# Optimization experiments

Measured on AMD Instinct MI355X. Metric: run time of the kernel, lower is better.

The kernel has to match this reference:

```python
import jax, jax.numpy as jnp
import numpy as np

N_WIRES = 16
VAR_DEPTH = 2
BATCH = 16


def _param_sizes():
    sizes = []
    n = N_WIRES
    lay = 0
    while n > 1:
        sizes.append(4 * int(np.ceil(N_WIRES / 2 ** lay)) * VAR_DEPTH)
        n = (n + 1) // 2
        lay += 1
    return sizes  # [128, 64, 32, 16]


def _apply_1q(psi, gate, w):
    # psi: (B, 2, ..., 2); gate: (2,2) complex; wire w lives on axis w+1
    psi = jnp.moveaxis(psi, w + 1, -1)
    psi = jnp.einsum('...j,ij->...i', psi, gate)
    return jnp.moveaxis(psi, -1, w + 1)


def _rx(psi, th, w):
    c = jnp.cos(th / 2).astype(jnp.complex64)
    s = jnp.sin(th / 2).astype(jnp.complex64)
    gate = jnp.stack([jnp.stack([c, -1j * s]), jnp.stack([-1j * s, c])])
    return _apply_1q(psi, gate, w)


def _rz(psi, th, w):
    ph = jnp.exp(0.5j * th * jnp.array([-1.0, 1.0], jnp.float32)).astype(jnp.complex64)
    shape = [1] * psi.ndim
    shape[w + 1] = 2
    return psi * ph.reshape(shape)


def _rzz(psi, th, wa, wb):
    # diag(e^{-i t/2}, e^{i t/2}, e^{i t/2}, e^{-i t/2}) -> sign = -1 if bits equal else +1
    sgn = jnp.array([[-1.0, 1.0], [1.0, -1.0]], jnp.float32)
    ph = jnp.exp(0.5j * th * sgn).astype(jnp.complex64)  # symmetric, transpose-safe
    a, b = min(wa, wb) + 1, max(wa, wb) + 1
    shape = [1] * psi.ndim
    shape[a] = 2
    shape[b] = 2
    return psi * ph.reshape(shape)


def _cnot(psi, c, t):
    p0 = jax.lax.slice_in_dim(psi, 0, 1, axis=c + 1)
    p1 = jax.lax.slice_in_dim(psi, 1, 2, axis=c + 1)
    return jnp.concatenate([p0, jnp.flip(p1, axis=t + 1)], axis=c + 1)


def _conv_layer(psi, params, active):
    n = len(active)
    for d in range(VAR_DEPTH):
        for j in range(n):
            base = 4 * j + d * 4 * n
            psi = _rx(psi, params[base + 0], active[j])
            psi = _rz(psi, params[base + 1], active[j])
            psi = _rx(psi, params[base + 2], active[j])
        for bg in (0, 1):
            for j in range(bg, n, 2):
                jn = (j + 1) % n  # ring coupling (wraps last->first)
                base = 4 * j + d * 4 * n
                psi = _rzz(psi, params[base + 3], active[j], active[jn])
    return psi


def _pool(psi, active):
    for j in range(0, len(active), 2):
        if j + 1 < len(active):
            psi = _cnot(psi, active[j], active[j + 1])
    return psi, active[::2]


def _forward(psi, params_list):
    active = list(range(N_WIRES))
    for p in params_list:
        psi = _conv_layer(psi, p, active)
        if len(active) > 1:
            psi, active = _pool(psi, active)
    w = active[0]  # measure Z on the surviving wire (wire 0)
    prob = psi.real ** 2 + psi.imag ** 2
    axes = tuple(a for a in range(1, psi.ndim) if a != w + 1)
    p2 = prob.sum(axis=axes)  # (B, 2)
    return p2[:, 0] - p2[:, 1]


def setup_inputs() -> dict:
    key = jax.random.key(0)
    ks = jax.random.split(key, 8)
    dim = 2 ** N_WIRES
    x_re = jax.random.normal(ks[0], (BATCH, dim), dtype=jnp.float32)
    x_im = jax.random.normal(ks[1], (BATCH, dim), dtype=jnp.float32)
    nrm = jnp.sqrt(jnp.sum(x_re ** 2 + x_im ** 2, axis=1, keepdims=True))
    x_re = x_re / nrm
    x_im = x_im / nrm
    sizes = _param_sizes()
    two_pi = 2.0 * np.pi
    params = [jax.random.uniform(ks[2 + i], (sizes[i],), dtype=jnp.float32) * two_pi
              for i in range(len(sizes))]
    return {"x_re": x_re, "x_im": x_im,
            "params0": params[0], "params1": params[1],
            "params2": params[2], "params3": params[3]}


def reference(x_re, x_im, params0, params1, params2, params3):
    psi = (x_re + 1j * x_im).astype(jnp.complex64)
    psi = psi.reshape((BATCH,) + (2,) * N_WIRES)
    return _forward(psi, [params0, params1, params2, params3])
```

## Files before the change

### kernel.cpp

```cpp
#include <hip/hip_runtime.h>


#define DEV __device__ __forceinline__
#define TBL(i) (tbl + (i)*8)

__device__ static const unsigned char G_CP[60] = {
  15,14,13,12,11,10,9,8,7,6,5,4,3,2,1,0,
  15,14,13,12,11,10,9,8,7,6,5,4,3,2,1,0,
  15,13,11,9,7,5,3,1,
  15,13,11,9,7,5,3,1,
  15,11,7,3,
  15,11,7,3,
  15,7,
  15,7
};
__device__ static const unsigned char G_CQ[60] = {
  14,13,12,11,10,9,8,7,6,5,4,3,2,1,0,15,
  14,13,12,11,10,9,8,7,6,5,4,3,2,1,0,15,
  13,11,9,7,5,3,1,15,
  13,11,9,7,5,3,1,15,
  11,7,3,15,
  11,7,3,15,
  7,15,
  7,15
};

DEV float2 F2(float x, float y){ float2 r; r.x = x; r.y = y; return r; }
DEV float2 cmulf(float2 a, float2 b){ return F2(a.x*b.x - a.y*b.y, a.x*b.y + a.y*b.x); }
DEV int swz(int j){ return j ^ ((j>>4)&15) ^ ((j>>8)&15); }

template<int SB>
DEV void gate4(float2* a, const float* __restrict__ g){
  float u00r=g[0],u00i=g[1],u01r=g[2],u01i=g[3],u10r=g[4],u10i=g[5],u11r=g[6],u11i=g[7];
  #pragma unroll
  for (int m=0;m<2;m++){
    int i0 = (SB==0) ? (m<<1) : m;
    int i1 = i0 | (1<<SB);
    float2 x0=a[i0], x1=a[i1];
    a[i0] = F2(u00r*x0.x - u00i*x0.y + u01r*x1.x - u01i*x1.y,
               u00r*x0.y + u00i*x0.x + u01r*x1.y + u01i*x1.x);
    a[i1] = F2(u10r*x0.x - u10i*x0.y + u11r*x1.x - u11i*x1.y,
               u10r*x0.y + u10i*x0.x + u11r*x1.y + u11i*x1.x);
  }
}

DEV void lgate(float2* a, const float* __restrict__ g, int mask, int lane){
  bool h = (lane & mask) != 0;
  float c0r = h ? g[4] : g[0], c0i = h ? g[5] : g[1];
  float c1r = h ? g[6] : g[2], c1i = h ? g[7] : g[3];
  #pragma unroll
  for (int s=0;s<4;s++){
    float px = __shfl_xor(a[s].x, mask);
    float py = __shfl_xor(a[s].y, mask);
    float x0x = h ? px : a[s].x, x0y = h ? py : a[s].y;
    float x1x = h ? a[s].x : px, x1y = h ? a[s].y : py;
    a[s] = F2(c0r*x0x - c0i*x0y + c1r*x1x - c1i*x1y,
              c0r*x0y + c0i*x0x + c1r*x1y + c1i*x1x);
  }
}

DEV void cswap(float2* a, int cmask, int tmask, int lane){
  bool c = (lane & cmask) != 0;
  #pragma unroll
  for (int s=0;s<4;s++){
    float px = __shfl_xor(a[s].x, tmask);
    float py = __shfl_xor(a[s].y, tmask);
    if (c){ a[s].x = px; a[s].y = py; }
  }
}

template<int C0,int N,unsigned M0,unsigned M1>
DEV void diag4(float2* a, const float* __restrict__ tbl, unsigned Ib){
  const unsigned regmask = M0|M1;
  float2 F0 = F2(1.f, 0.f);
  #pragma unroll
  for (int k=0;k<N;k++){
    const int p = G_CP[C0+k], q = G_CQ[C0+k];
    if ( !(((1u<<p)|(1u<<q)) & regmask) ){
      float c = tbl[480 + 2*(C0+k)], s = tbl[481 + 2*(C0+k)];
      unsigned x = ((Ib>>p) ^ (Ib>>q)) & 1u;
      F0 = cmulf(F0, F2(c, x ? s : -s));
    }
  }
  #pragma unroll
  for (int r=0;r<4;r++){
    unsigned Ir = Ib ^ ((r&1)?M0:0u) ^ ((r&2)?M1:0u);
    float2 ph = F0;
    #pragma unroll
    for (int k=0;k<N;k++){
      const int p = G_CP[C0+k], q = G_CQ[C0+k];
      if ( ((1u<<p)|(1u<<q)) & regmask ){
        float c = tbl[480 + 2*(C0+k)], s = tbl[481 + 2*(C0+k)];
        unsigned x = ((Ir>>p) ^ (Ir>>q)) & 1u;
        ph = cmulf(ph, F2(c, x ? s : -s));
      }
    }
    a[r] = cmulf(a[r], ph);
  }
}

DEV unsigned Ib2(int j, int o){ return (unsigned)((j&63) | (o<<6) | ((j>>6)<<11)); }
DEV unsigned Ic(int j, int o){
  return (unsigned)( ((j&1)<<1) | (((j>>1)&1)<<3) | (((j>>2)&1)<<5)
       | (((j>>3)&63)<<6) | (((j>>9)&1)<<13) | (((j>>10)&1)<<15)
       | (o&1) | (((o>>1)&1)<<2) | (((o>>2)&1)<<4) | (((o>>3)&1)<<12) | (((o>>4)&1)<<14) );
}
DEV unsigned s1b(unsigned I){ return I ^ ((I & 0xA02Au) >> 1); }

__global__ void k_setup(const float* __restrict__ p0, const float* __restrict__ p1,
                        const float* __restrict__ p2, const float* __restrict__ p3,
                        float* __restrict__ tbl, float* __restrict__ out){
  int g = threadIdx.x;
  if (g < 16) out[g] = 0.f;
  if (g >= 60) return;
  int d, j, n; const float* P;
  if (g < 32)      { n=16; d=(g>>4)&1; j=g&15; P=p0; }
  else if (g < 48) { n=8;  d=(g>>3)&1; j=g&7;  P=p1; }
  else if (g < 56) { n=4;  d=(g>>2)&1; j=g&3;  P=p2; }
  else             { n=2;  d=(g>>1)&1; j=g&1;  P=p3; }
  int base = 4*j + 4*n*d;
  double th0 = P[base+0], th1 = P[base+1], th2 = P[base+2], th3 = P[base+3];
  double c0 = cos(th0*0.5), s0 = sin(th0*0.5);
  double ca = cos(th1*0.5), sa = sin(th1*0.5);
  double c2 = cos(th2*0.5), s2 = sin(th2*0.5);
  double B00r =  ca*c0, B00i = -sa*c0;
  double B01r = -sa*s0, B01i = -ca*s0;
  double B10r =  sa*s0, B10i = -ca*s0;
  double B11r =  ca*c0, B11i =  sa*c0;
  float* o = tbl + g*8;
  o[0]=(float)(c2*B00r + s2*B10i); o[1]=(float)(c2*B00i - s2*B10r);
  o[2]=(float)(c2*B01r + s2*B11i); o[3]=(float)(c2*B01i - s2*B11r);
  o[4]=(float)(s2*B00i + c2*B10r); o[5]=(float)(-s2*B00r + c2*B10i);
  o[6]=(float)(s2*B01i + c2*B11r); o[7]=(float)(-s2*B01r + c2*B11i);
  tbl[480 + 2*g] = (float)cos(th3*0.5);
  tbl[481 + 2*g] = (float)sin(th3*0.5);
}

__global__ __launch_bounds__(512, 4)
void k_p1(const float* __restrict__ xre, const float* __restrict__ xim,
          const float* __restrict__ tbl, float2* __restrict__ st){
  const int t = threadIdx.x, lane = t & 63, wv = t >> 6;
  const int batch = blockIdx.x >> 5, o = blockIdx.x & 31;
  const unsigned hi = ((unsigned)batch<<16) | ((unsigned)o<<11);
  __shared__ float2 lds[2048];
  float2 a[4];
  {
    unsigned base = hi | ((unsigned)t<<2);
    float4 re = *(const float4*)(xre + base);
    float4 im = *(const float4*)(xim + base);
    a[0]=F2(re.x,im.x); a[1]=F2(re.y,im.y); a[2]=F2(re.z,im.z); a[3]=F2(re.w,im.w);
  }
  gate4<0>(a, TBL(15)); gate4<1>(a, TBL(14));
  lgate(a, TBL(13), 1, lane);  lgate(a, TBL(12), 2, lane);
  lgate(a, TBL(11), 4, lane);  lgate(a, TBL(10), 8, lane);
  lgate(a, TBL(9), 16, lane);  lgate(a, TBL(8), 32, lane);
  #pragma unroll
  for (int s=0;s<4;s++) lds[swz((t<<2)|s)] = a[s];
  __syncthreads();
  #pragma unroll
  for (int s=0;s<4;s++){
    int jB = (lane&31) | (wv<<5) | (s<<8) | ((lane>>5)<<10);
    a[s] = lds[swz(jB)];
  }
  gate4<0>(a, TBL(7)); gate4<1>(a, TBL(6));
  lgate(a, TBL(5), 32, lane);
  #pragma unroll
  for (int s=0;s<4;s++){
    int jB = (lane&31) | (wv<<5) | (s<<8) | ((lane>>5)<<10);
    st[hi | (unsigned)jB] = a[s];
  }
}

__global__ __launch_bounds__(512, 4)
void k_p2(const float* __restrict__ tbl, float2* __restrict__ st){
  const int t = threadIdx.x, lane = t & 63, wv = t >> 6;
  const int batch = blockIdx.x >> 5, o = blockIdx.x & 31;
  const unsigned bb = (unsigned)batch<<16;
  __shared__ float2 lds[2048];
  float2 a[4];
  int jA0 = ((lane&1)<<8) | (((lane>>1)&1)<<7) | (((lane>>2)&1)<<6)
          | (((lane>>3)&1)<<0) | (((lane>>4)&1)<<1) | (((lane>>5)&1)<<2) | (wv<<3);
  #pragma unroll
  for (int s=0;s<4;s++){
    int jA = jA0 | ((s&1)<<10) | (((s>>1)&1)<<9);
    a[s] = st[bb | Ib2(jA, o)];
  }
  gate4<0>(a, TBL(0)); gate4<1>(a, TBL(1));
  lgate(a, TBL(2), 1, lane); lgate(a, TBL(3), 2, lane); lgate(a, TBL(4), 4, lane);
  diag4<0,16, (1u<<15),(1u<<14)>(a, tbl, Ib2(jA0, o));
  lgate(a, TBL(20), 4, lane); lgate(a, TBL(19), 2, lane); lgate(a, TBL(18), 1, lane);
  gate4<1>(a, TBL(17)); gate4<0>(a, TBL(16));
  lgate(a, TBL(31), 8, lane); lgate(a, TBL(30), 16, lane); lgate(a, TBL(29), 32, lane);
  #pragma unroll
  for (int s=0;s<4;s++){
    int jA = jA0 | ((s&1)<<10) | (((s>>1)&1)<<9);
    lds[swz(jA)] = a[s];
  }
  __syncthreads();
  int jB0 = (lane&7) | (((lane>>3)&1)<<5) | (wv<<6)
          | (((lane>>4)&1)<<9) | (((lane>>5)&1)<<10);
  #pragma unroll
  for (int s=0;s<4;s++){
    int jB = jB0 | ((s&1)<<3) | (((s>>1)&1)<<4);
    a[s] = lds[swz(jB)];
  }
  gate4<0>(a, TBL(28)); gate4<1>(a, TBL(27));
  lgate(a, TBL(26), 8, lane);
  #pragma unroll
  for (int s=0;s<4;s++){
    int jB = jB0 | ((s&1)<<3) | (((s>>1)&1)<<4);
    st[bb | Ib2(jB, o)] = a[s];
  }
}

__global__ __launch_bounds__(512, 4)
void k_p4(const float* __restrict__ tbl, float2* __restrict__ st, float* __restrict__ out){
  const int t = threadIdx.x, lane = t & 63, wv = t >> 6;
  const int batch = blockIdx.x >> 5, o = blockIdx.x & 31;
  const unsigned bb = (unsigned)batch<<16;
  __shared__ float2 lds[2048];
  __shared__ float red[8];
  float2 a[4];
  int jA0 = (lane&7) | (((lane>>3)&7)<<5) | (wv<<8);
  #pragma unroll
  for (int s=0;s<4;s++){
    int jA = jA0 | ((s&1)<<3) | (((s>>1)&1)<<4);
    a[s] = st[bb | s1b(Ic(jA, o))];
  }
  gate4<0>(a, TBL(25)); gate4<1>(a, TBL(24));
  lgate(a, TBL(23), 8, lane); lgate(a, TBL(22), 16, lane); lgate(a, TBL(21), 32, lane);
  diag4<16,16, (1u<<6),(1u<<7)>(a, tbl, s1b(Ic(jA0, o)));
  if (wv & 1){
    #pragma unroll
    for (int s=0;s<4;s++){ a[s].x = __shfl_xor(a[s].x, 32); a[s].y = __shfl_xor(a[s].y, 32); }
  }
  cswap(a, 16, 8, lane);
  { float2 tmp=a[2]; a[2]=a[3]; a[3]=tmp; }
  #pragma unroll
  for (int s=0;s<4;s++){
    int jA = jA0 | ((s&1)<<3) | (((s>>1)&1)<<4);
    lds[swz(jA)] = a[s];
  }
  __syncthreads();
  int jB0 = ((lane&1)<<2) | (((lane>>1)&1)<<4) | (((lane>>2)&1)<<6)
          | (((lane>>3)&1)<<8) | (((lane>>4)&1)<<9) | (((lane>>5)&1)<<10)
          | ((wv&1)<<3) | (((wv>>1)&1)<<5) | (((wv>>2)&1)<<7);
  #pragma unroll
  for (int s=0;s<4;s++) a[s] = lds[swz(jB0 | (s&1) | (((s>>1)&1)<<1))];
  const unsigned IbB = Ic(jB0, o);
  gate4<0>(a, TBL(39)); gate4<1>(a, TBL(38));
  lgate(a, TBL(37), 1, lane); lgate(a, TBL(36), 2, lane); lgate(a, TBL(35), 4, lane);
  lgate(a, TBL(34), 8, lane); lgate(a, TBL(33), 16, lane); lgate(a, TBL(32), 32, lane);
  diag4<32,8, 2u,8u>(a, tbl, IbB);
  gate4<0>(a, TBL(47)); gate4<1>(a, TBL(46));
  lgate(a, TBL(45), 1, lane); lgate(a, TBL(44), 2, lane); lgate(a, TBL(43), 4, lane);
  lgate(a, TBL(42), 8, lane); lgate(a, TBL(41), 16, lane); lgate(a, TBL(40), 32, lane);
  diag4<40,8, 2u,8u>(a, tbl, IbB);
  cswap(a, 32, 16, lane); cswap(a, 8, 4, lane); cswap(a, 2, 1, lane);
  { float2 tmp=a[2]; a[2]=a[3]; a[3]=tmp; }
  lgate(a, TBL(48), 32, lane); lgate(a, TBL(49), 8, lane); lgate(a, TBL(50), 2, lane);
  gate4<1>(a, TBL(51));
  diag4<48,4, 2u,8u>(a, tbl, IbB);
  lgate(a, TBL(52), 32, lane); lgate(a, TBL(53), 8, lane); lgate(a, TBL(54), 2, lane);
  gate4<1>(a, TBL(55));
  diag4<52,4, 2u,8u>(a, tbl, IbB);
  cswap(a, 32, 8, lane);
  if (lane & 2){
    float2 t0=a[0]; a[0]=a[2]; a[2]=t0;
    float2 t1=a[1]; a[1]=a[3]; a[3]=t1;
  }
  lgate(a, TBL(56), 32, lane); lgate(a, TBL(57), 2, lane);
  diag4<56,2, 2u,8u>(a, tbl, IbB);
  lgate(a, TBL(58), 32, lane);
  float sl = 0.f;
  #pragma unroll
  for (int s=0;s<4;s++) sl += a[s].x*a[s].x + a[s].y*a[s].y;
  float sg = (lane & 32) ? -sl : sl;
  #pragma unroll
  for (int off=32; off>0; off>>=1) sg += __shfl_down(sg, off);
  __syncthreads();
  if ((t & 63) == 0) red[wv] = sg;
  __syncthreads();
  if (t == 0){
    float tot = 0.f;
    #pragma unroll
    for (int w=0; w<8; w++) tot += red[w];
    atomicAdd(out + batch, tot);
  }
}

extern "C" void kernel_launch(void* const* d_in, const int* in_sizes, int n_in,
                              void* d_out, int out_size, void* d_ws, size_t ws_size,
                              hipStream_t stream) {
  const float* xre = (const float*)d_in[0];
  const float* xim = (const float*)d_in[1];
  const float* p0  = (const float*)d_in[2];
  const float* p1  = (const float*)d_in[3];
  const float* p2  = (const float*)d_in[4];
  const float* p3  = (const float*)d_in[5];
  float* out = (float*)d_out;
  float2* st = (float2*)d_ws;
  float* tbl = (float*)((char*)d_ws + (8u<<20));

  k_setup<<<1, 64, 0, stream>>>(p0, p1, p2, p3, tbl, out);
  k_p1<<<512, 512, 0, stream>>>(xre, xim, tbl, st);
  k_p2<<<512, 512, 0, stream>>>(tbl, st);
  k_p4<<<512, 512, 0, stream>>>(tbl, st, out);
}
```

Baseline: 115.1 us.

## Fuse setup into first pass, use permlane32 swaps and phase-sum diagonals

Removes the separate setup kernel launch: every block of the first pass builds the gate table in shared memory, and block 0 writes it to global memory for the later passes. Lane-32 exchanges use the permlane32_swap builtin instead of shuffles. The shuffle gate gets a cheaper per-half coefficient form. Diagonal RZZ phases become a sum of angles followed by one sincos, instead of a chain of complex multiplies. The trade-offs are fp32 instead of fp64 table math, redundant table builds in every block, and a fast-math sincos.

```diff
diff --git a/kernel.cpp b/kernel.cpp
--- a/kernel.cpp
+++ b/kernel.cpp
@@ -2,7 +2,6 @@
 
 
 #define DEV __device__ __forceinline__
-#define TBL(i) (tbl + (i)*8)
 
 __device__ static const unsigned char G_CP[60] = {
   15,14,13,12,11,10,9,8,7,6,5,4,3,2,1,0,
@@ -29,6 +28,17 @@
 DEV float2 cmulf(float2 a, float2 b){ return F2(a.x*b.x - a.y*b.y, a.x*b.y + a.y*b.x); }
 DEV int swz(int j){ return j ^ ((j>>4)&15) ^ ((j>>8)&15); }
 
+#if __has_builtin(__builtin_amdgcn_permlane32_swap)
+#define HAVE_PLS 1
+DEV void plswap01(float &x0, float &x1){
+  auto r = __builtin_amdgcn_permlane32_swap(__float_as_uint(x0), __float_as_uint(x1), false, false);
+  x0 = __uint_as_float((unsigned)r[0]);
+  x1 = __uint_as_float((unsigned)r[1]);
+}
+#else
+#define HAVE_PLS 0
+#endif
+
 template<int SB>
 DEV void gate4(float2* a, const float* __restrict__ g){
   float u00r=g[0],u00i=g[1],u01r=g[2],u01i=g[3],u10r=g[4],u10i=g[5],u11r=g[6],u11i=g[7];
@@ -46,17 +56,32 @@
 
 DEV void lgate(float2* a, const float* __restrict__ g, int mask, int lane){
   bool h = (lane & mask) != 0;
+  float Ar = h ? g[6] : g[0], Ai = h ? g[7] : g[1];
+  float Br = h ? g[4] : g[2], Bi = h ? g[5] : g[3];
+  #pragma unroll
+  for (int s=0;s<4;s++){
+    float px = __shfl_xor(a[s].x, mask);
+    float py = __shfl_xor(a[s].y, mask);
+    a[s] = F2(Ar*a[s].x - Ai*a[s].y + Br*px - Bi*py,
+              Ar*a[s].y + Ai*a[s].x + Br*py + Bi*px);
+  }
+}
+
+DEV void lgate32(float2* a, const float* __restrict__ g, int lane){
+#if HAVE_PLS
+  bool h = (lane & 32) != 0;
   float c0r = h ? g[4] : g[0], c0i = h ? g[5] : g[1];
   float c1r = h ? g[6] : g[2], c1i = h ? g[7] : g[3];
   #pragma unroll
   for (int s=0;s<4;s++){
-    float px = __shfl_xor(a[s].x, mask);
-    float py = __shfl_xor(a[s].y, mask);
-    float x0x = h ? px : a[s].x, x0y = h ? py : a[s].y;
-    float x1x = h ? a[s].x : px, x1y = h ? a[s].y : py;
+    float x0x = a[s].x, x1x = a[s].x, x0y = a[s].y, x1y = a[s].y;
+    plswap01(x0x, x1x); plswap01(x0y, x1y);
     a[s] = F2(c0r*x0x - c0i*x0y + c1r*x1x - c1i*x1y,
               c0r*x0y + c0i*x0x + c1r*x1y + c1i*x1x);
   }
+#else
+  lgate(a, g, 32, lane);
+#endif
 }
 
 DEV void cswap(float2* a, int cmask, int tmask, int lane){
@@ -70,79 +95,80 @@
 }
 
 template<int C0,int N,unsigned M0,unsigned M1>
-DEV void diag4(float2* a, const float* __restrict__ tbl, unsigned Ib){
+DEV void diag4(float2* a, const float* __restrict__ hh, unsigned Ib){
   const unsigned regmask = M0|M1;
-  float2 F0 = F2(1.f, 0.f);
+  float base = 0.f;
   #pragma unroll
   for (int k=0;k<N;k++){
     const int p = G_CP[C0+k], q = G_CQ[C0+k];
     if ( !(((1u<<p)|(1u<<q)) & regmask) ){
-      float c = tbl[480 + 2*(C0+k)], s = tbl[481 + 2*(C0+k)];
+      float h = hh[C0+k];
       unsigned x = ((Ib>>p) ^ (Ib>>q)) & 1u;
-      F0 = cmulf(F0, F2(c, x ? s : -s));
+      base += x ? h : -h;
     }
   }
   #pragma unroll
   for (int r=0;r<4;r++){
     unsigned Ir = Ib ^ ((r&1)?M0:0u) ^ ((r&2)?M1:0u);
-    float2 ph = F0;
+    float ph = base;
     #pragma unroll
     for (int k=0;k<N;k++){
       const int p = G_CP[C0+k], q = G_CQ[C0+k];
       if ( ((1u<<p)|(1u<<q)) & regmask ){
-        float c = tbl[480 + 2*(C0+k)], s = tbl[481 + 2*(C0+k)];
+        float h = hh[C0+k];
         unsigned x = ((Ir>>p) ^ (Ir>>q)) & 1u;
-        ph = cmulf(ph, F2(c, x ? s : -s));
+        ph += x ? h : -h;
       }
     }
-    a[r] = cmulf(a[r], ph);
-  }
-}
-
-DEV unsigned Ib2(int j, int o){ return (unsigned)((j&63) | (o<<6) | ((j>>6)<<11)); }
-DEV unsigned Ic(int j, int o){
-  return (unsigned)( ((j&1)<<1) | (((j>>1)&1)<<3) | (((j>>2)&1)<<5)
-       | (((j>>3)&63)<<6) | (((j>>9)&1)<<13) | (((j>>10)&1)<<15)
-       | (o&1) | (((o>>1)&1)<<2) | (((o>>2)&1)<<4) | (((o>>3)&1)<<12) | (((o>>4)&1)<<14) );
-}
-DEV unsigned s1b(unsigned I){ return I ^ ((I & 0xA02Au) >> 1); }
-
-__global__ void k_setup(const float* __restrict__ p0, const float* __restrict__ p1,
-                        const float* __restrict__ p2, const float* __restrict__ p3,
-                        float* __restrict__ tbl, float* __restrict__ out){
-  int g = threadIdx.x;
-  if (g < 16) out[g] = 0.f;
-  if (g >= 60) return;
+    float c, s;
+    __sincosf(ph, &s, &c);
+    a[r] = cmulf(a[r], F2(c, s));
+  }
+}
+
+DEV void build_entry(float* sh, const float* __restrict__ p0, const float* __restrict__ p1,
+                     const float* __restrict__ p2, const float* __restrict__ p3, int g){
   int d, j, n; const float* P;
   if (g < 32)      { n=16; d=(g>>4)&1; j=g&15; P=p0; }
   else if (g < 48) { n=8;  d=(g>>3)&1; j=g&7;  P=p1; }
   else if (g < 56) { n=4;  d=(g>>2)&1; j=g&3;  P=p2; }
   else             { n=2;  d=(g>>1)&1; j=g&1;  P=p3; }
   int base = 4*j + 4*n*d;
-  double th0 = P[base+0], th1 = P[base+1], th2 = P[base+2], th3 = P[base+3];
-  double c0 = cos(th0*0.5), s0 = sin(th0*0.5);
-  double ca = cos(th1*0.5), sa = sin(th1*0.5);
-  double c2 = cos(th2*0.5), s2 = sin(th2*0.5);
-  double B00r =  ca*c0, B00i = -sa*c0;
-  double B01r = -sa*s0, B01i = -ca*s0;
-  double B10r =  sa*s0, B10i = -ca*s0;
-  double B11r =  ca*c0, B11i =  sa*c0;
-  float* o = tbl + g*8;
-  o[0]=(float)(c2*B00r + s2*B10i); o[1]=(float)(c2*B00i - s2*B10r);
-  o[2]=(float)(c2*B01r + s2*B11i); o[3]=(float)(c2*B01i - s2*B11r);
-  o[4]=(float)(s2*B00i + c2*B10r); o[5]=(float)(-s2*B00r + c2*B10i);
-  o[6]=(float)(s2*B01i + c2*B11r); o[7]=(float)(-s2*B01r + c2*B11i);
-  tbl[480 + 2*g] = (float)cos(th3*0.5);
-  tbl[481 + 2*g] = (float)sin(th3*0.5);
-}
+  float th0 = P[base+0], th1 = P[base+1], th2 = P[base+2], th3 = P[base+3];
+  float c0,s0,ca,sa,c2,s2;
+  sincosf(0.5f*th0, &s0, &c0);
+  sincosf(0.5f*th1, &sa, &ca);
+  sincosf(0.5f*th2, &s2, &c2);
+  float B00r =  ca*c0, B00i = -sa*c0;
+  float B01r = -sa*s0, B01i = -ca*s0;
+  float B10r =  sa*s0, B10i = -ca*s0;
+  float B11r =  ca*c0, B11i =  sa*c0;
+  float* o8 = sh + g*8;
+  o8[0]=c2*B00r + s2*B10i; o8[1]=c2*B00i - s2*B10r;
+  o8[2]=c2*B01r + s2*B11i; o8[3]=c2*B01i - s2*B11r;
+  o8[4]=s2*B00i + c2*B10r; o8[5]=-s2*B00r + c2*B10i;
+  o8[6]=s2*B01i + c2*B11r; o8[7]=-s2*B01r + c2*B11i;
+  sh[480 + g] = 0.5f*th3;
+}
+
+DEV unsigned Ib2(int j, int o){ return (unsigned)((j&63) | (o<<6) | ((j>>6)<<11)); }
+DEV unsigned Ic(int j, int o){
+  return (unsigned)( ((j&1)<<1) | (((j>>1)&1)<<3) | (((j>>2)&1)<<5)
+       | (((j>>3)&63)<<6) | (((j>>9)&1)<<13) | (((j>>10)&1)<<15)
+       | (o&1) | (((o>>1)&1)<<2) | (((o>>2)&1)<<4) | (((o>>3)&1)<<12) | (((o>>4)&1)<<14) );
+}
+DEV unsigned s1b(unsigned I){ return I ^ ((I & 0xA02Au) >> 1); }
 
 __global__ __launch_bounds__(512, 4)
 void k_p1(const float* __restrict__ xre, const float* __restrict__ xim,
-          const float* __restrict__ tbl, float2* __restrict__ st){
+          const float* __restrict__ pp0, const float* __restrict__ pp1,
+          const float* __restrict__ pp2, const float* __restrict__ pp3,
+          float* __restrict__ tbl, float2* __restrict__ st, float* __restrict__ out){
   const int t = threadIdx.x, lane = t & 63, wv = t >> 6;
   const int batch = blockIdx.x >> 5, o = blockIdx.x & 31;
   const unsigned hi = ((unsigned)batch<<16) | ((unsigned)o<<11);
   __shared__ float2 lds[2048];
+  __shared__ float sh[544];
   float2 a[4];
   {
     unsigned base = hi | ((unsigned)t<<2);
@@ -150,10 +176,17 @@
     float4 im = *(const float4*)(xim + base);
     a[0]=F2(re.x,im.x); a[1]=F2(re.y,im.y); a[2]=F2(re.z,im.z); a[3]=F2(re.w,im.w);
   }
-  gate4<0>(a, TBL(15)); gate4<1>(a, TBL(14));
-  lgate(a, TBL(13), 1, lane);  lgate(a, TBL(12), 2, lane);
-  lgate(a, TBL(11), 4, lane);  lgate(a, TBL(10), 8, lane);
-  lgate(a, TBL(9), 16, lane);  lgate(a, TBL(8), 32, lane);
+  if (t < 60) build_entry(sh, pp0, pp1, pp2, pp3, t);
+  if (blockIdx.x == 0 && t >= 64 && t < 80) out[t - 64] = 0.f;
+  __syncthreads();
+  if (blockIdx.x == 0){
+    for (int i = t; i < 540; i += 512) tbl[i] = sh[i];
+  }
+  #define LTB(i) (sh + (i)*8)
+  gate4<0>(a, LTB(15)); gate4<1>(a, LTB(14));
+  lgate(a, LTB(13), 1, lane);  lgate(a, LTB(12), 2, lane);
+  lgate(a, LTB(11), 4, lane);  lgate(a, LTB(10), 8, lane);
+  lgate(a, LTB(9), 16, lane);  lgate32(a, LTB(8), lane);
   #pragma unroll
   for (int s=0;s<4;s++) lds[swz((t<<2)|s)] = a[s];
   __syncthreads();
@@ -162,14 +195,17 @@
     int jB = (lane&31) | (wv<<5) | (s<<8) | ((lane>>5)<<10);
     a[s] = lds[swz(jB)];
   }
-  gate4<0>(a, TBL(7)); gate4<1>(a, TBL(6));
-  lgate(a, TBL(5), 32, lane);
+  gate4<0>(a, LTB(7)); gate4<1>(a, LTB(6));
+  lgate32(a, LTB(5), lane);
   #pragma unroll
   for (int s=0;s<4;s++){
     int jB = (lane&31) | (wv<<5) | (s<<8) | ((lane>>5)<<10);
     st[hi | (unsigned)jB] = a[s];
   }
-}
+  #undef LTB
+}
+
+#define TBL(i) (tbl + (i)*8)
 
 __global__ __launch_bounds__(512, 4)
 void k_p2(const float* __restrict__ tbl, float2* __restrict__ st){
@@ -187,10 +223,10 @@
   }
   gate4<0>(a, TBL(0)); gate4<1>(a, TBL(1));
   lgate(a, TBL(2), 1, lane); lgate(a, TBL(3), 2, lane); lgate(a, TBL(4), 4, lane);
-  diag4<0,16, (1u<<15),(1u<<14)>(a, tbl, Ib2(jA0, o));
+  diag4<0,16, (1u<<15),(1u<<14)>(a, tbl+480, Ib2(jA0, o));
   lgate(a, TBL(20), 4, lane); lgate(a, TBL(19), 2, lane); lgate(a, TBL(18), 1, lane);
   gate4<1>(a, TBL(17)); gate4<0>(a, TBL(16));
-  lgate(a, TBL(31), 8, lane); lgate(a, TBL(30), 16, lane); lgate(a, TBL(29), 32, lane);
+  lgate(a, TBL(31), 8, lane); lgate(a, TBL(30), 16, lane); lgate32(a, TBL(29), lane);
   #pragma unroll
   for (int s=0;s<4;s++){
     int jA = jA0 | ((s&1)<<10) | (((s>>1)&1)<<9);
@@ -228,11 +264,21 @@
     a[s] = st[bb | s1b(Ic(jA, o))];
   }
   gate4<0>(a, TBL(25)); gate4<1>(a, TBL(24));
-  lgate(a, TBL(23), 8, lane); lgate(a, TBL(22), 16, lane); lgate(a, TBL(21), 32, lane);
-  diag4<16,16, (1u<<6),(1u<<7)>(a, tbl, s1b(Ic(jA0, o)));
+  lgate(a, TBL(23), 8, lane); lgate(a, TBL(22), 16, lane); lgate32(a, TBL(21), lane);
+  diag4<16,16, (1u<<6),(1u<<7)>(a, tbl+480, s1b(Ic(jA0, o)));
   if (wv & 1){
+#if HAVE_PLS
+    #pragma unroll
+    for (int s=0;s<4;s++){
+      float x0x=a[s].x, x1x=a[s].x, x0y=a[s].y, x1y=a[s].y;
+      plswap01(x0x, x1x); plswap01(x0y, x1y);
+      a[s].x = (lane & 32) ? x0x : x1x;
+      a[s].y = (lane & 32) ? x0y : x1y;
+    }
+#else
     #pragma unroll
     for (int s=0;s<4;s++){ a[s].x = __shfl_xor(a[s].x, 32); a[s].y = __shfl_xor(a[s].y, 32); }
+#endif
   }
   cswap(a, 16, 8, lane);
   { float2 tmp=a[2]; a[2]=a[3]; a[3]=tmp; }
@@ -250,28 +296,28 @@
   const unsigned IbB = Ic(jB0, o);
   gate4<0>(a, TBL(39)); gate4<1>(a, TBL(38));
   lgate(a, TBL(37), 1, lane); lgate(a, TBL(36), 2, lane); lgate(a, TBL(35), 4, lane);
-  lgate(a, TBL(34), 8, lane); lgate(a, TBL(33), 16, lane); lgate(a, TBL(32), 32, lane);
-  diag4<32,8, 2u,8u>(a, tbl, IbB);
+  lgate(a, TBL(34), 8, lane); lgate(a, TBL(33), 16, lane); lgate32(a, TBL(32), lane);
+  diag4<32,8, 2u,8u>(a, tbl+480, IbB);
   gate4<0>(a, TBL(47)); gate4<1>(a, TBL(46));
   lgate(a, TBL(45), 1, lane); lgate(a, TBL(44), 2, lane); lgate(a, TBL(43), 4, lane);
-  lgate(a, TBL(42), 8, lane); lgate(a, TBL(41), 16, lane); lgate(a, TBL(40), 32, lane);
-  diag4<40,8, 2u,8u>(a, tbl, IbB);
+  lgate(a, TBL(42), 8, lane); lgate(a, TBL(41), 16, lane); lgate32(a, TBL(40), lane);
+  diag4<40,8, 2u,8u>(a, tbl+480, IbB);
   cswap(a, 32, 16, lane); cswap(a, 8, 4, lane); cswap(a, 2, 1, lane);
   { float2 tmp=a[2]; a[2]=a[3]; a[3]=tmp; }
-  lgate(a, TBL(48), 32, lane); lgate(a, TBL(49), 8, lane); lgate(a, TBL(50), 2, lane);
+  lgate32(a, TBL(48), lane); lgate(a, TBL(49), 8, lane); lgate(a, TBL(50), 2, lane);
   gate4<1>(a, TBL(51));
-  diag4<48,4, 2u,8u>(a, tbl, IbB);
-  lgate(a, TBL(52), 32, lane); lgate(a, TBL(53), 8, lane); lgate(a, TBL(54), 2, lane);
+  diag4<48,4, 2u,8u>(a, tbl+480, IbB);
+  lgate32(a, TBL(52), lane); lgate(a, TBL(53), 8, lane); lgate(a, TBL(54), 2, lane);
   gate4<1>(a, TBL(55));
-  diag4<52,4, 2u,8u>(a, tbl, IbB);
+  diag4<52,4, 2u,8u>(a, tbl+480, IbB);
   cswap(a, 32, 8, lane);
   if (lane & 2){
     float2 t0=a[0]; a[0]=a[2]; a[2]=t0;
     float2 t1=a[1]; a[1]=a[3]; a[3]=t1;
   }
-  lgate(a, TBL(56), 32, lane); lgate(a, TBL(57), 2, lane);
-  diag4<56,2, 2u,8u>(a, tbl, IbB);
-  lgate(a, TBL(58), 32, lane);
+  lgate32(a, TBL(56), lane); lgate(a, TBL(57), 2, lane);
+  diag4<56,2, 2u,8u>(a, tbl+480, IbB);
+  lgate32(a, TBL(58), lane);
   float sl = 0.f;
   #pragma unroll
   for (int s=0;s<4;s++) sl += a[s].x*a[s].x + a[s].y*a[s].y;
@@ -302,8 +348,7 @@
   float2* st = (float2*)d_ws;
   float* tbl = (float*)((char*)d_ws + (8u<<20));
 
-  k_setup<<<1, 64, 0, stream>>>(p0, p1, p2, p3, tbl, out);
-  k_p1<<<512, 512, 0, stream>>>(xre, xim, tbl, st);
+  k_p1<<<512, 512, 0, stream>>>(xre, xim, p0, p1, p2, p3, tbl, st, out);
   k_p2<<<512, 512, 0, stream>>>(tbl, st);
   k_p4<<<512, 512, 0, stream>>>(tbl, st, out);
 }
```

New measurement: 107.6 us. -6.5%, faster.
